# Kernel optimization log

Measured on AMD Instinct MI355X. Metric: run time of the kernel, lower is better.

## Reference

```python
import jax, jax.numpy as jnp
import numpy as np

NEG = jnp.float32(-1e10)

def setup_inputs() -> dict:
    key = jax.random.key(0)
    k1, k2, k3, k4 = jax.random.split(key, 4)
    B, Ns, Nr, D = 64, 512, 256, 1024
    return {
        "span_embeddings": jax.random.normal(k1, (B, Ns, D), dtype=jnp.float32),
        "image_embeddings": jax.random.normal(k2, (B, Nr, D), dtype=jnp.float32),
        "span_mask": jax.random.randint(k3, (B, Ns), 0, 2).astype(jnp.int32),
        "image_mask": jax.random.randint(k4, (B, Nr), 0, 2).astype(jnp.int32),
    }

def reference(span_embeddings, image_embeddings, span_mask, image_mask):
    # pair mask: (B, Ns, Nr) = image_mask[b, None, r] * span_mask[b, s, None]
    mask = (image_mask[:, None, :] * span_mask[:, :, None]).astype(span_embeddings.dtype)
    # QK^T with multiplicative mask, then custom zero->-1e10 masking
    att = jnp.einsum('bsd,brd->bsr', span_embeddings, image_embeddings) * mask
    att = jnp.where(att != 0, att, NEG)
    # spans attend over ROIs
    w_first = jax.nn.softmax(att, axis=-1) * mask
    att_first = jnp.einsum('bsr,brd->bsd', w_first, image_embeddings)
    score = jnp.mean(jnp.square(span_embeddings - att_first))
    # ROIs attend over spans (score_type='both')
    att_t = jnp.swapaxes(att, 1, 2)            # (B, Nr, Ns)
    w_second = jax.nn.softmax(att_t, axis=-1) * jnp.swapaxes(mask, 1, 2)
    att_second = jnp.einsum('brs,bsd->brd', w_second, span_embeddings)
    score = score + jnp.mean(jnp.square(image_embeddings - att_second))
    return score, att_first, att
```

## Files before the change

### kernel.cpp

```cpp
#include <hip/hip_runtime.h>
#include <hip/hip_bf16.h>
#include <math.h>

#define B_  64
#define NS  512
#define NR  256
#define DD  1024
#define NEGV (-1e10f)

typedef __attribute__((ext_vector_type(4))) float f32x4;
typedef __attribute__((ext_vector_type(8))) short bf16x8;

__device__ __forceinline__ unsigned short f2bf(float x) {
    unsigned u = __builtin_bit_cast(unsigned, x);
    unsigned r = u + 0x7FFFu + ((u >> 16) & 1u);
    return (unsigned short)(r >> 16);
}
__device__ __forceinline__ unsigned pk2(float x, float y) {
    unsigned r;
    asm("v_cvt_pk_bf16_f32 %0, %1, %2" : "=v"(r) : "v"(x), "v"(y));
    return r;
}
__device__ __forceinline__ void pk_hilo(float x, float y, unsigned& h, unsigned& l) {
    h = pk2(x, y);
    const float hx = __builtin_bit_cast(float, h << 16);
    const float hy = __builtin_bit_cast(float, h & 0xFFFF0000u);
    l = pk2(x - hx, y - hy);
}
__device__ __forceinline__ void gload16(const void* g, void* l) {
    __builtin_amdgcn_global_load_lds((const __attribute__((address_space(1))) void*)g,
                                     (__attribute__((address_space(3))) void*)l, 16, 0, 0);
}

__global__ __launch_bounds__(64) void zero_ws(double* ws) {
    if (threadIdx.x == 0) { ws[0] = 0.0; ws[1] = 0.0; }
}

__global__ __launch_bounds__(512) void att_mfma(
    const float* __restrict__ span, const float* __restrict__ image,
    const int* __restrict__ smask, const int* __restrict__ imask,
    float* __restrict__ att, float2* __restrict__ rowP, float2* __restrict__ colP,
    int doStats) {
    const int id = blockIdx.x;
    const int b  = id & 63;
    const int ys = (id >> 6) & 3;
    const int xr = id >> 8;
    const int s0 = ys * 128;
    const int r0 = xr * 128;
    __shared__ unsigned short Ah[128][40], Al[128][40], Bh[128][40], Bl[128][40];
    const int tid  = threadIdx.x;
    const int lane = tid & 63;
    const int w    = tid >> 6;
    const int wso  = (w >> 2) * 64;
    const int wro  = (w & 3) * 32;
    const float* Sp = span  + ((size_t)b * NS + s0) * DD;
    const float* Im = image + ((size_t)b * NR + r0) * DD;

    f32x4 acc[4][2];
    #pragma unroll
    for (int i = 0; i < 4; ++i)
        #pragma unroll
        for (int j = 0; j < 2; ++j) acc[i][j] = (f32x4){0.f, 0.f, 0.f, 0.f};

    const int row0 = tid >> 2;
    const int kq   = (tid & 3) * 8;
    const int fr   = lane & 15;
    const int fq   = lane >> 4;
    const int fk   = fq * 8;

    for (int k0 = 0; k0 < DD; k0 += 32) {
        {
            const float4 a0 = *reinterpret_cast<const float4*>(Sp + (size_t)row0 * DD + k0 + kq);
            const float4 a1 = *reinterpret_cast<const float4*>(Sp + (size_t)row0 * DD + k0 + kq + 4);
            const float4 c0 = *reinterpret_cast<const float4*>(Im + (size_t)row0 * DD + k0 + kq);
            const float4 c1 = *reinterpret_cast<const float4*>(Im + (size_t)row0 * DD + k0 + kq + 4);
            unsigned h0, l0, h1, l1, h2, l2, h3, l3;
            uint4 u;
            pk_hilo(a0.x, a0.y, h0, l0); pk_hilo(a0.z, a0.w, h1, l1);
            pk_hilo(a1.x, a1.y, h2, l2); pk_hilo(a1.z, a1.w, h3, l3);
            u.x = h0; u.y = h1; u.z = h2; u.w = h3;
            *reinterpret_cast<uint4*>(&Ah[row0][kq]) = u;
            u.x = l0; u.y = l1; u.z = l2; u.w = l3;
            *reinterpret_cast<uint4*>(&Al[row0][kq]) = u;
            pk_hilo(c0.x, c0.y, h0, l0); pk_hilo(c0.z, c0.w, h1, l1);
            pk_hilo(c1.x, c1.y, h2, l2); pk_hilo(c1.z, c1.w, h3, l3);
            u.x = h0; u.y = h1; u.z = h2; u.w = h3;
            *reinterpret_cast<uint4*>(&Bh[row0][kq]) = u;
            u.x = l0; u.y = l1; u.z = l2; u.w = l3;
            *reinterpret_cast<uint4*>(&Bl[row0][kq]) = u;
        }
        __syncthreads();
        bf16x8 ah[4], al[4], bh[2], bl[2];
        #pragma unroll
        for (int mf = 0; mf < 4; ++mf) {
            ah[mf] = *reinterpret_cast<const bf16x8*>(&Ah[wso + mf * 16 + fr][fk]);
            al[mf] = *reinterpret_cast<const bf16x8*>(&Al[wso + mf * 16 + fr][fk]);
        }
        #pragma unroll
        for (int nf = 0; nf < 2; ++nf) {
            bh[nf] = *reinterpret_cast<const bf16x8*>(&Bh[wro + nf * 16 + fr][fk]);
            bl[nf] = *reinterpret_cast<const bf16x8*>(&Bl[wro + nf * 16 + fr][fk]);
        }
        #pragma unroll
        for (int mf = 0; mf < 4; ++mf)
            #pragma unroll
            for (int nf = 0; nf < 2; ++nf) {
                acc[mf][nf] = __builtin_amdgcn_mfma_f32_16x16x32_bf16(ah[mf], bh[nf], acc[mf][nf], 0, 0, 0);
                acc[mf][nf] = __builtin_amdgcn_mfma_f32_16x16x32_bf16(ah[mf], bl[nf], acc[mf][nf], 0, 0, 0);
                acc[mf][nf] = __builtin_amdgcn_mfma_f32_16x16x32_bf16(al[mf], bh[nf], acc[mf][nf], 0, 0, 0);
            }
        __syncthreads();
    }

    float2* rowLDS = reinterpret_cast<float2*>(&Ah[0][0]);
    float2* colLDS = rowLDS + 512;
    int imv[2];
    #pragma unroll
    for (int nf = 0; nf < 2; ++nf) imv[nf] = imask[b * NR + r0 + wro + nf * 16 + fr];
    float cmax[2] = {-3.4e38f, -3.4e38f};
    float smv[4][4];
    #pragma unroll
    for (int mf = 0; mf < 4; ++mf) {
        #pragma unroll
        for (int i = 0; i < 4; ++i) {
            const int s = s0 + wso + mf * 16 + fq * 4 + i;
            const int sm = smask[b * NS + s];
            smv[mf][i] = (float)sm;
            float* orow = att + ((size_t)b * NS + s) * NR + r0 + wro;
            float vj[2];
            #pragma unroll
            for (int nf = 0; nf < 2; ++nf) {
                float v = acc[mf][nf][i] * (float)(sm * imv[nf]);
                v = (v != 0.0f) ? v : NEGV;
                orow[nf * 16 + fr] = v;
                vj[nf] = v;
                cmax[nf] = fmaxf(cmax[nf], v);
            }
            if (doStats) {
                float rm = fmaxf(vj[0], vj[1]);
                rm = fmaxf(rm, __shfl_xor(rm, 1));
                rm = fmaxf(rm, __shfl_xor(rm, 2));
                rm = fmaxf(rm, __shfl_xor(rm, 4));
                rm = fmaxf(rm, __shfl_xor(rm, 8));
                float rs = __expf(vj[0] - rm) + __expf(vj[1] - rm);
                rs += __shfl_xor(rs, 1);
                rs += __shfl_xor(rs, 2);
                rs += __shfl_xor(rs, 4);
                rs += __shfl_xor(rs, 8);
                if (fr == 0) rowLDS[(wso + mf * 16 + fq * 4 + i) * 4 + (w & 3)] = make_float2(rm, rs);
            }
        }
    }
    if (doStats) {
        #pragma unroll
        for (int nf = 0; nf < 2; ++nf) {
            cmax[nf] = fmaxf(cmax[nf], __shfl_xor(cmax[nf], 16));
            cmax[nf] = fmaxf(cmax[nf], __shfl_xor(cmax[nf], 32));
        }
        float csum[2] = {0.f, 0.f};
        #pragma unroll
        for (int mf = 0; mf < 4; ++mf)
            #pragma unroll
            for (int i = 0; i < 4; ++i)
                #pragma unroll
                for (int nf = 0; nf < 2; ++nf) {
                    float v = acc[mf][nf][i] * (smv[mf][i] * (float)imv[nf]);
                    v = (v != 0.0f) ? v : NEGV;
                    csum[nf] += __expf(v - cmax[nf]);
                }
        #pragma unroll
        for (int nf = 0; nf < 2; ++nf) {
            csum[nf] += __shfl_xor(csum[nf], 16);
            csum[nf] += __shfl_xor(csum[nf], 32);
        }
        if (lane < 16) {
            #pragma unroll
            for (int nf = 0; nf < 2; ++nf)
                colLDS[(wro + nf * 16 + lane) * 2 + (w >> 2)] = make_float2(cmax[nf], csum[nf]);
        }
        __syncthreads();
        if (tid < 128) {
            float2 q0 = rowLDS[tid * 4 + 0], q1 = rowLDS[tid * 4 + 1];
            float2 q2 = rowLDS[tid * 4 + 2], q3 = rowLDS[tid * 4 + 3];
            const float m = fmaxf(fmaxf(q0.x, q1.x), fmaxf(q2.x, q3.x));
            const float ssum = q0.y * __expf(q0.x - m) + q1.y * __expf(q1.x - m)
                             + q2.y * __expf(q2.x - m) + q3.y * __expf(q3.x - m);
            rowP[((size_t)b * NS + s0 + tid) * 2 + xr] = make_float2(m, ssum);
        } else if (tid < 256) {
            const int c = tid - 128;
            const float2 q0 = colLDS[c * 2 + 0], q1 = colLDS[c * 2 + 1];
            const float m = fmaxf(q0.x, q1.x);
            const float ssum = q0.y * __expf(q0.x - m) + q1.y * __expf(q1.x - m);
            colP[((size_t)b * NR + r0 + c) * 4 + ys] = make_float2(m, ssum);
        }
    }
}

__global__ __launch_bounds__(256) void combine_stats(
    const float2* __restrict__ rowP, const float2* __restrict__ colP,
    const int* __restrict__ smask, const int* __restrict__ imask,
    float* __restrict__ m1, float* __restrict__ f1,
    float* __restrict__ m2, float* __restrict__ f2) {
    const int idx = blockIdx.x * 256 + threadIdx.x;
    if (idx < B_ * NS) {
        const float2 p0 = rowP[(size_t)idx * 2 + 0];
        const float2 p1 = rowP[(size_t)idx * 2 + 1];
        const float m = fmaxf(p0.x, p1.x);
        const float s = p0.y * __expf(p0.x - m) + p1.y * __expf(p1.x - m);
        m1[idx] = m;
        f1[idx] = (float)smask[idx] / s;
    } else if (idx < B_ * NS + B_ * NR) {
        const int j = idx - B_ * NS;
        const float2 p0 = colP[(size_t)j * 4 + 0];
        const float2 p1 = colP[(size_t)j * 4 + 1];
        const float2 p2 = colP[(size_t)j * 4 + 2];
        const float2 p3 = colP[(size_t)j * 4 + 3];
        const float m = fmaxf(fmaxf(p0.x, p1.x), fmaxf(p2.x, p3.x));
        const float s = p0.y * __expf(p0.x - m) + p1.y * __expf(p1.x - m)
                      + p2.y * __expf(p2.x - m) + p3.y * __expf(p3.x - m);
        m2[j] = m;
        f2[j] = (float)imask[j] / s;
    }
}

__global__ __launch_bounds__(256) void transpose_swz(
    const float* __restrict__ src, unsigned short* __restrict__ dst, int N) {
    const int b = blockIdx.z, n0 = blockIdx.y * 32, d0 = blockIdx.x * 32;
    __shared__ unsigned short T[32][36];
    const int t = threadIdx.x;
    {
        const int n = t >> 3, dq = (t & 7) * 4;
        const float4 v = *reinterpret_cast<const float4*>(src + ((size_t)b * N + n0 + n) * DD + d0 + dq);
        T[dq + 0][n] = f2bf(v.x); T[dq + 1][n] = f2bf(v.y);
        T[dq + 2][n] = f2bf(v.z); T[dq + 3][n] = f2bf(v.w);
    }
    __syncthreads();
    {
        const int d = t >> 3, nq = (t & 7) * 4;
        const int dg = d0 + d;
        const int base = n0 + nq;
        const int pos = (base & 63) ^ ((dg & 7) << 3);
        const size_t idx = ((size_t)b * DD + dg) * N + (base & ~63) + pos;
        *reinterpret_cast<ushort4*>(dst + idx) = *reinterpret_cast<const ushort4*>(&T[d][nq]);
    }
}

__global__ __launch_bounds__(256) void build_w12(
    const float* __restrict__ att, const int* __restrict__ smask,
    const int* __restrict__ imask,
    const float* __restrict__ m1, const float* __restrict__ f1,
    const float* __restrict__ m2, const float* __restrict__ f2,
    unsigned short* __restrict__ w1g, unsigned short* __restrict__ w2g) {
    const int b = blockIdx.z, s0 = blockIdx.y * 64, r0 = blockIdx.x * 64;
    __shared__ unsigned short T[64][68];
    __shared__ float m2s[64], f2s[64], ims[64];
    const int tid = threadIdx.x;
    if (tid < 64) {
        m2s[tid] = m2[b * NR + r0 + tid];
        f2s[tid] = f2[b * NR + r0 + tid];
        ims[tid] = (float)imask[b * NR + r0 + tid];
    }
    __syncthreads();
    {
        const int srow = tid >> 2, rg = (tid & 3) * 16;
        const int s = s0 + srow;
        const float m1v = m1[b * NS + s], f1v = f1[b * NS + s];
        const float smv = (float)smask[b * NS + s];
        const float* arow = att + ((size_t)b * NS + s) * NR + r0;
        const int w1swz = (s & 7) << 3;
        unsigned short* w1row = w1g + ((size_t)b * NS + s) * NR + r0;
        #pragma unroll
        for (int g = 0; g < 4; ++g) {
            const int rr = rg + g * 4;
            const float4 a = *reinterpret_cast<const float4*>(arow + rr);
            const float e0 = __expf(a.x - m1v) * f1v * ims[rr + 0];
            const float e1 = __expf(a.y - m1v) * f1v * ims[rr + 1];
            const float e2 = __expf(a.z - m1v) * f1v * ims[rr + 2];
            const float e3 = __expf(a.w - m1v) * f1v * ims[rr + 3];
            uint2 u; u.x = pk2(e0, e1); u.y = pk2(e2, e3);
            *reinterpret_cast<uint2*>(w1row + (rr ^ w1swz)) = u;
            const float q0 = __expf(a.x - m2s[rr + 0]) * f2s[rr + 0] * smv;
            const float q1 = __expf(a.y - m2s[rr + 1]) * f2s[rr + 1] * smv;
            const float q2 = __expf(a.z - m2s[rr + 2]) * f2s[rr + 2] * smv;
            const float q3 = __expf(a.w - m2s[rr + 3]) * f2s[rr + 3] * smv;
            const unsigned t0 = pk2(q0, q1), t1 = pk2(q2, q3);
            T[rr + 0][srow] = (unsigned short)(t0 & 0xFFFF);
            T[rr + 1][srow] = (unsigned short)(t0 >> 16);
            T[rr + 2][srow] = (unsigned short)(t1 & 0xFFFF);
            T[rr + 3][srow] = (unsigned short)(t1 >> 16);
        }
    }
    __syncthreads();
    {
        const int rl = tid >> 2, sg = (tid & 3) * 16;
        const int w2swz = (rl & 7) << 3;
        unsigned short* w2row = w2g + ((size_t)b * NR + r0 + rl) * NS + s0;
        #pragma unroll
        for (int g = 0; g < 4; ++g) {
            const int ss = sg + g * 4;
            *reinterpret_cast<ushort4*>(w2row + (ss ^ w2swz)) =
                *reinterpret_cast<const ushort4*>(&T[rl][ss]);
        }
    }
}

template<int KTOT, int MT, bool WOUT, int WIDX>
__global__ __launch_bounds__(256) void gemm_apply(
    const unsigned short* __restrict__ Ag, const unsigned short* __restrict__ Btg,
    const float* __restrict__ ref, float* __restrict__ outp, double* __restrict__ wsum) {
    const int b = blockIdx.z, m0 = blockIdx.y * 64, d0 = blockIdx.x * 256;
    __shared__ unsigned short As[64 * 64];
    __shared__ unsigned short Bs[256 * 64];
    __shared__ float redsum[256];
    const int tid = threadIdx.x, lane = tid & 63, w = tid >> 6;
    const int fr = lane & 15, fq = lane >> 4;
    f32x4 acc[4][4];
    #pragma unroll
    for (int i = 0; i < 4; ++i)
        #pragma unroll
        for (int j = 0; j < 4; ++j) acc[i][j] = (f32x4){0.f, 0.f, 0.f, 0.f};

    const int srow = tid >> 3;
    const int scol = (tid & 7) * 16;
    for (int kc = 0; kc < KTOT / 64; ++kc) {
        const char* asrc = (const char*)(Ag + ((size_t)b * MT + m0) * KTOT) + kc * 128 + scol;
        #pragma unroll
        for (int c = 0; c < 2; ++c)
            gload16(asrc + (size_t)(c * 32 + srow) * (KTOT * 2), (char*)As + (c * 256 + tid) * 16);
        const char* bsrc = (const char*)(Btg + ((size_t)b * DD + d0) * KTOT) + kc * 128 + scol;
        #pragma unroll
        for (int c = 0; c < 8; ++c)
            gload16(bsrc + (size_t)(c * 32 + srow) * (KTOT * 2), (char*)Bs + (c * 256 + tid) * 16);
        __syncthreads();
        #pragma unroll
        for (int ks = 0; ks < 2; ++ks) {
            bf16x8 aF[4], bF[4];
            #pragma unroll
            for (int mf = 0; mf < 4; ++mf) {
                const int row = mf * 16 + fr;
                const int pos = (ks * 32 + fq * 8) ^ ((row & 7) << 3);
                aF[mf] = *reinterpret_cast<const bf16x8*>(&As[row * 64 + pos]);
            }
            #pragma unroll
            for (int nf = 0; nf < 4; ++nf) {
                const int row = w * 64 + nf * 16 + fr;
                const int pos = (ks * 32 + fq * 8) ^ ((row & 7) << 3);
                bF[nf] = *reinterpret_cast<const bf16x8*>(&Bs[row * 64 + pos]);
            }
            #pragma unroll
            for (int mf = 0; mf < 4; ++mf)
                #pragma unroll
                for (int nf = 0; nf < 4; ++nf)
                    acc[mf][nf] = __builtin_amdgcn_mfma_f32_16x16x32_bf16(aF[mf], bF[nf], acc[mf][nf], 0, 0, 0);
        }
        __syncthreads();
    }
    float sumsq = 0.0f;
    #pragma unroll
    for (int mf = 0; mf < 4; ++mf) {
        #pragma unroll
        for (int i = 0; i < 4; ++i) {
            const int row = m0 + mf * 16 + fq * 4 + i;
            const size_t base = ((size_t)b * MT + row) * DD + d0 + w * 64;
            #pragma unroll
            for (int nf = 0; nf < 4; ++nf) {
                const float v = acc[mf][nf][i];
                const float rv = ref[base + nf * 16 + fr];
                if constexpr (WOUT) outp[base + nf * 16 + fr] = v;
                const float dx = rv - v;
                sumsq += dx * dx;
            }
        }
    }
    redsum[tid] = sumsq; __syncthreads();
    for (int off = 128; off; off >>= 1) {
        if (tid < off) redsum[tid] += redsum[tid + off];
        __syncthreads();
    }
    if (tid == 0) atomicAdd(wsum + WIDX, (double)redsum[0]);
}

__global__ __launch_bounds__(256) void first_kernel(
    const float* __restrict__ span, const float* __restrict__ image,
    const int* __restrict__ smask, const int* __restrict__ imask,
    const float* __restrict__ att, float* __restrict__ att_first,
    double* __restrict__ ws) {
    const int b  = blockIdx.y;
    const int s0 = blockIdx.x * 32;
    __shared__ float wT[256][36];
    __shared__ float Is[32][132];
    __shared__ float red[256];
    const int tid  = threadIdx.x;
    const int lane = tid & 63, wave = tid >> 6;
    for (int i = 0; i < 8; ++i) {
        const int srel = wave * 8 + i;
        const int s    = s0 + srel;
        const float4 v = *reinterpret_cast<const float4*>(att + ((size_t)b * NS + s) * NR + lane * 4);
        float m = fmaxf(fmaxf(v.x, v.y), fmaxf(v.z, v.w));
        #pragma unroll
        for (int off = 32; off; off >>= 1) m = fmaxf(m, __shfl_xor(m, off));
        float4 e;
        e.x = expf(v.x - m); e.y = expf(v.y - m); e.z = expf(v.z - m); e.w = expf(v.w - m);
        float sum = e.x + e.y + e.z + e.w;
        #pragma unroll
        for (int off = 32; off; off >>= 1) sum += __shfl_xor(sum, off);
        const float fac = (float)smask[b * NS + s] / sum;
        const int4 im4 = *reinterpret_cast<const int4*>(imask + b * NR + lane * 4);
        wT[lane * 4 + 0][srel] = e.x * fac * (float)im4.x;
        wT[lane * 4 + 1][srel] = e.y * fac * (float)im4.y;
        wT[lane * 4 + 2][srel] = e.z * fac * (float)im4.z;
        wT[lane * 4 + 3][srel] = e.w * fac * (float)im4.w;
    }
    __syncthreads();
    float sumsq = 0.0f;
    const int txd = tid & 31;
    const int tys = tid >> 5;
    const float* Ib = image + (size_t)b * NR * DD;
    for (int dc = 0; dc < 8; ++dc) {
        const int d0 = dc * 128;
        float acc[4][4] = {};
        for (int rc = 0; rc < 8; ++rc) {
            const int r0 = rc * 32;
            {
                const int rr = tid >> 3;
                const int cb = tid & 7;
                const float* src = Ib + (size_t)(r0 + rr) * DD + d0;
                #pragma unroll
                for (int q = 0; q < 4; ++q)
                    *reinterpret_cast<float4*>(&Is[rr][(cb + 8 * q) * 4]) =
                        *reinterpret_cast<const float4*>(src + (cb + 8 * q) * 4);
            }
            __syncthreads();
            #pragma unroll 4
            for (int rr = 0; rr < 32; ++rr) {
                const float4 wv = *reinterpret_cast<const float4*>(&wT[r0 + rr][tys * 4]);
                const float4 iv = *reinterpret_cast<const float4*>(&Is[rr][txd * 4]);
                const float wvv[4] = {wv.x, wv.y, wv.z, wv.w};
                const float ivv[4] = {iv.x, iv.y, iv.z, iv.w};
                #pragma unroll
                for (int i = 0; i < 4; ++i)
                    #pragma unroll
                    for (int j = 0; j < 4; ++j)
                        acc[i][j] += wvv[i] * ivv[j];
            }
            __syncthreads();
        }
        #pragma unroll
        for (int i = 0; i < 4; ++i) {
            const int s = s0 + tys * 4 + i;
            const size_t base = ((size_t)b * NS + s) * DD + d0 + txd * 4;
            const float4 af = {acc[i][0], acc[i][1], acc[i][2], acc[i][3]};
            *reinterpret_cast<float4*>(att_first + base) = af;
            const float4 sp = *reinterpret_cast<const float4*>(span + base);
            float dx;
            dx = sp.x - af.x; sumsq += dx * dx;
            dx = sp.y - af.y; sumsq += dx * dx;
            dx = sp.z - af.z; sumsq += dx * dx;
            dx = sp.w - af.w; sumsq += dx * dx;
        }
    }
    red[tid] = sumsq; __syncthreads();
    for (int off = 128; off; off >>= 1) {
        if (tid < off) red[tid] += red[tid + off];
        __syncthreads();
    }
    if (tid == 0) atomicAdd(ws, (double)red[0]);
}

__global__ __launch_bounds__(256) void second_kernel(
    const float* __restrict__ span, const float* __restrict__ image,
    const int* __restrict__ smask, const int* __restrict__ imask,
    const float* __restrict__ att, double* __restrict__ ws) {
    const int b  = blockIdx.y;
    const int r0 = blockIdx.x * 32;
    __shared__ float w2s[32][36];
    __shared__ float Ss[32][132];
    __shared__ float mArr[32], fArr[32];
    __shared__ float redm[8][32];
    __shared__ float red[256];
    const int tid = threadIdx.x;
    const int rr = tid & 31, q = tid >> 5;
    const float* attb = att + (size_t)b * NS * NR + r0 + rr;
    float mloc = -3.4e38f;
    for (int t = 0; t < 64; ++t)
        mloc = fmaxf(mloc, attb[(size_t)(q * 64 + t) * NR]);
    redm[q][rr] = mloc;
    __syncthreads();
    if (tid < 32) {
        float m = redm[0][tid];
        #pragma unroll
        for (int qq = 1; qq < 8; ++qq) m = fmaxf(m, redm[qq][tid]);
        mArr[tid] = m;
    }
    __syncthreads();
    const float mcol = mArr[rr];
    float sloc = 0.0f;
    for (int t = 0; t < 64; ++t)
        sloc += expf(attb[(size_t)(q * 64 + t) * NR] - mcol);
    redm[q][rr] = sloc;
    __syncthreads();
    if (tid < 32) {
        float s = 0.0f;
        #pragma unroll
        for (int qq = 0; qq < 8; ++qq) s += redm[qq][tid];
        fArr[tid] = (float)imask[b * NR + r0 + tid] / s;
    }
    __syncthreads();
    float sumsq = 0.0f;
    const int txd = tid & 31;
    const int tyr = tid >> 5;
    const float* Sb = span + (size_t)b * NS * DD;
    for (int dc = 0; dc < 8; ++dc) {
        const int d0 = dc * 128;
        float acc[4][4] = {};
        for (int sc = 0; sc < 16; ++sc) {
            const int sb0 = sc * 32;
            {
                const int sr = tid >> 3;
                const int cb = tid & 7;
                const float* src = Sb + (size_t)(sb0 + sr) * DD + d0;
                #pragma unroll
                for (int qq = 0; qq < 4; ++qq)
                    *reinterpret_cast<float4*>(&Ss[sr][(cb + 8 * qq) * 4]) =
                        *reinterpret_cast<const float4*>(src + (cb + 8 * qq) * 4);
            }
            {
                const int ss = tid >> 3;
                const int rq = (tid & 7) * 4;
                const int s  = sb0 + ss;
                const float4 v = *reinterpret_cast<const float4*>(att + ((size_t)b * NS + s) * NR + r0 + rq);
                const float smv = (float)smask[b * NS + s];
                float4 wv;
                wv.x = expf(v.x - mArr[rq + 0]) * fArr[rq + 0] * smv;
                wv.y = expf(v.y - mArr[rq + 1]) * fArr[rq + 1] * smv;
                wv.z = expf(v.z - mArr[rq + 2]) * fArr[rq + 2] * smv;
                wv.w = expf(v.w - mArr[rq + 3]) * fArr[rq + 3] * smv;
                *reinterpret_cast<float4*>(&w2s[ss][rq]) = wv;
            }
            __syncthreads();
            #pragma unroll 4
            for (int ss = 0; ss < 32; ++ss) {
                const float4 wv = *reinterpret_cast<const float4*>(&w2s[ss][tyr * 4]);
                const float4 sv = *reinterpret_cast<const float4*>(&Ss[ss][txd * 4]);
                const float wvv[4] = {wv.x, wv.y, wv.z, wv.w};
                const float svv[4] = {sv.x, sv.y, sv.z, sv.w};
                #pragma unroll
                for (int i = 0; i < 4; ++i)
                    #pragma unroll
                    for (int j = 0; j < 4; ++j)
                        acc[i][j] += wvv[i] * svv[j];
            }
            __syncthreads();
        }
        #pragma unroll
        for (int i = 0; i < 4; ++i) {
            const int r = r0 + tyr * 4 + i;
            const float4 iv = *reinterpret_cast<const float4*>(image + ((size_t)b * NR + r) * DD + d0 + txd * 4);
            float dx;
            dx = iv.x - acc[i][0]; sumsq += dx * dx;
            dx = iv.y - acc[i][1]; sumsq += dx * dx;
            dx = iv.z - acc[i][2]; sumsq += dx * dx;
            dx = iv.w - acc[i][3]; sumsq += dx * dx;
        }
    }
    red[tid] = sumsq; __syncthreads();
    for (int off = 128; off; off >>= 1) {
        if (tid < off) red[tid] += red[tid + off];
        __syncthreads();
    }
    if (tid == 0) atomicAdd(ws + 1, (double)red[0]);
}

__global__ __launch_bounds__(64) void score_kernel(const double* __restrict__ ws, float* __restrict__ out) {
    if (threadIdx.x == 0) {
        out[0] = (float)(ws[0] / (double)((size_t)B_ * NS * DD) +
                         ws[1] / (double)((size_t)B_ * NR * DD));
    }
}

extern "C" void kernel_launch(void* const* d_in, const int* in_sizes, int n_in,
                              void* d_out, int out_size, void* d_ws, size_t ws_size,
                              hipStream_t stream) {
    const float* span  = (const float*)d_in[0];
    const float* image = (const float*)d_in[1];
    const int*   smask = (const int*)d_in[2];
    const int*   imask = (const int*)d_in[3];
    float* out       = (float*)d_out;
    float* att_first = out + 1;
    float* att       = out + 1 + (size_t)B_ * NS * DD;

    char* base = (char*)d_ws;
    double* wsum = (double*)base;
    float* m1 = (float*)(base + 512);
    float* f1 = m1 + (size_t)B_ * NS;
    float* m2 = f1 + (size_t)B_ * NS;
    float* f2 = m2 + (size_t)B_ * NR;
    float2* rowP = (float2*)(f2 + (size_t)B_ * NR);
    float2* colP = rowP + (size_t)B_ * NS * 2;
    char* X0 = (char*)(colP + (size_t)B_ * NR * 4);
    unsigned short* imgT = (unsigned short*)X0;
    unsigned short* w1g  = (unsigned short*)(X0 + (size_t)B_ * DD * NR * 2);
    unsigned short* spT  = (unsigned short*)X0;
    unsigned short* w2g  = (unsigned short*)(X0 + (size_t)B_ * DD * NS * 2);
    const size_t NEED = (size_t)(X0 - base) + (size_t)B_ * DD * NS * 2 + (size_t)B_ * NS * NR * 2;
    const int wsok = (ws_size >= NEED) ? 1 : 0;

    zero_ws<<<dim3(1), dim3(64), 0, stream>>>(wsum);
    att_mfma<<<dim3(512), dim3(512), 0, stream>>>(
        span, image, smask, imask, att, rowP, colP, wsok);

    if (wsok) {
        combine_stats<<<dim3((B_ * NS + B_ * NR) / 256), dim3(256), 0, stream>>>(
            rowP, colP, smask, imask, m1, f1, m2, f2);
        transpose_swz<<<dim3(DD / 32, NR / 32, B_), dim3(256), 0, stream>>>(image, imgT, NR);
        build_w12<<<dim3(NR / 64, NS / 64, B_), dim3(256), 0, stream>>>(
            att, smask, imask, m1, f1, m2, f2, w1g, w2g);
        gemm_apply<NR, NS, true, 0><<<dim3(DD / 256, NS / 64, B_), dim3(256), 0, stream>>>(
            w1g, imgT, span, att_first, wsum);
        transpose_swz<<<dim3(DD / 32, NS / 32, B_), dim3(256), 0, stream>>>(span, spT, NS);
        gemm_apply<NS, NR, false, 1><<<dim3(DD / 256, NR / 64, B_), dim3(256), 0, stream>>>(
            w2g, spT, image, nullptr, wsum);
    } else {
        first_kernel<<<dim3(NS / 32, B_), dim3(256), 0, stream>>>(span, image, smask, imask, att, att_first, wsum);
        second_kernel<<<dim3(NR / 32, B_), dim3(256), 0, stream>>>(span, image, smask, imask, att, wsum);
    }
    score_kernel<<<dim3(1), dim3(64), 0, stream>>>(wsum, out);
}
```

Baseline: 297.3 us.

## Merge prep stages and both apply GEMMs into two combined launches

Folds the stats combine, both bf16 transposes and the weight build into one heterogeneous prep kernel, and runs the two apply GEMMs as a single grid whose blocks choose their problem by blockIdx.y. The per-row and per-column softmax stats are recomputed per tile in shared memory rather than written to global arrays. This removes several launches and the serialization between small kernels. In exchange the workspace grows, because the span and image transposes no longer share a buffer, and the stats are recomputed redundantly across tiles.

After: 290.9 us, median of 2. 2.2% less time.

```diff
diff --git a/kernel.cpp b/kernel.cpp
--- a/kernel.cpp
+++ b/kernel.cpp
@@ -7,6 +7,7 @@
 #define NR  256
 #define DD  1024
 #define NEGV (-1e10f)
+#define NTRANS (32 * 24 * B_)
 
 typedef __attribute__((ext_vector_type(4))) float f32x4;
 typedef __attribute__((ext_vector_type(8))) short bf16x8;
@@ -196,75 +197,73 @@
     }
 }
 
-__global__ __launch_bounds__(256) void combine_stats(
+__global__ __launch_bounds__(256) void prep_kernel(
+    const float* __restrict__ span, const float* __restrict__ image,
+    const int* __restrict__ smask, const int* __restrict__ imask,
+    const float* __restrict__ att,
     const float2* __restrict__ rowP, const float2* __restrict__ colP,
-    const int* __restrict__ smask, const int* __restrict__ imask,
-    float* __restrict__ m1, float* __restrict__ f1,
-    float* __restrict__ m2, float* __restrict__ f2) {
-    const int idx = blockIdx.x * 256 + threadIdx.x;
-    if (idx < B_ * NS) {
-        const float2 p0 = rowP[(size_t)idx * 2 + 0];
-        const float2 p1 = rowP[(size_t)idx * 2 + 1];
+    unsigned short* __restrict__ imgT, unsigned short* __restrict__ spT,
+    unsigned short* __restrict__ w1g, unsigned short* __restrict__ w2g) {
+    __shared__ unsigned short Tt[32][36];
+    __shared__ unsigned short Tb[64][68];
+    __shared__ float m1s[64], f1s[64], m2s[64], f2s[64], ims[64];
+    const int id  = blockIdx.x;
+    const int tid = threadIdx.x;
+    if (id < NTRANS) {
+        const int x = id & 31;
+        const int y = (id >> 5) % 24;
+        const int b = id / (32 * 24);
+        const int d0 = x * 32;
+        const float* src; unsigned short* dst; int N, n0;
+        if (y < 8) { src = image; dst = imgT; N = NR; n0 = y * 32; }
+        else       { src = span;  dst = spT;  N = NS; n0 = (y - 8) * 32; }
+        {
+            const int n = tid >> 3, dq = (tid & 7) * 4;
+            const float4 v = *reinterpret_cast<const float4*>(src + ((size_t)b * N + n0 + n) * DD + d0 + dq);
+            Tt[dq + 0][n] = f2bf(v.x); Tt[dq + 1][n] = f2bf(v.y);
+            Tt[dq + 2][n] = f2bf(v.z); Tt[dq + 3][n] = f2bf(v.w);
+        }
+        __syncthreads();
+        {
+            const int d = tid >> 3, nq = (tid & 7) * 4;
+            const int dg = d0 + d;
+            const int base = n0 + nq;
+            const int pos = (base & 63) ^ ((dg & 7) << 3);
+            const size_t idx = ((size_t)b * DD + dg) * N + (base & ~63) + pos;
+            *reinterpret_cast<ushort4*>(dst + idx) = *reinterpret_cast<const ushort4*>(&Tt[d][nq]);
+        }
+        return;
+    }
+    const int rem = id - NTRANS;
+    const int x = rem & 3;
+    const int y = (rem >> 2) & 7;
+    const int b = rem >> 5;
+    const int s0 = y * 64, r0 = x * 64;
+    if (tid < 64) {
+        const int gs = b * NS + s0 + tid;
+        const float2 p0 = rowP[(size_t)gs * 2 + 0];
+        const float2 p1 = rowP[(size_t)gs * 2 + 1];
         const float m = fmaxf(p0.x, p1.x);
-        const float s = p0.y * __expf(p0.x - m) + p1.y * __expf(p1.x - m);
-        m1[idx] = m;
-        f1[idx] = (float)smask[idx] / s;
-    } else if (idx < B_ * NS + B_ * NR) {
-        const int j = idx - B_ * NS;
-        const float2 p0 = colP[(size_t)j * 4 + 0];
-        const float2 p1 = colP[(size_t)j * 4 + 1];
-        const float2 p2 = colP[(size_t)j * 4 + 2];
-        const float2 p3 = colP[(size_t)j * 4 + 3];
-        const float m = fmaxf(fmaxf(p0.x, p1.x), fmaxf(p2.x, p3.x));
-        const float s = p0.y * __expf(p0.x - m) + p1.y * __expf(p1.x - m)
-                      + p2.y * __expf(p2.x - m) + p3.y * __expf(p3.x - m);
-        m2[j] = m;
-        f2[j] = (float)imask[j] / s;
-    }
-}
-
-__global__ __launch_bounds__(256) void transpose_swz(
-    const float* __restrict__ src, unsigned short* __restrict__ dst, int N) {
-    const int b = blockIdx.z, n0 = blockIdx.y * 32, d0 = blockIdx.x * 32;
-    __shared__ unsigned short T[32][36];
-    const int t = threadIdx.x;
-    {
-        const int n = t >> 3, dq = (t & 7) * 4;
-        const float4 v = *reinterpret_cast<const float4*>(src + ((size_t)b * N + n0 + n) * DD + d0 + dq);
-        T[dq + 0][n] = f2bf(v.x); T[dq + 1][n] = f2bf(v.y);
-        T[dq + 2][n] = f2bf(v.z); T[dq + 3][n] = f2bf(v.w);
-    }
-    __syncthreads();
-    {
-        const int d = t >> 3, nq = (t & 7) * 4;
-        const int dg = d0 + d;
-        const int base = n0 + nq;
-        const int pos = (base & 63) ^ ((dg & 7) << 3);
-        const size_t idx = ((size_t)b * DD + dg) * N + (base & ~63) + pos;
-        *reinterpret_cast<ushort4*>(dst + idx) = *reinterpret_cast<const ushort4*>(&T[d][nq]);
-    }
-}
-
-__global__ __launch_bounds__(256) void build_w12(
-    const float* __restrict__ att, const int* __restrict__ smask,
-    const int* __restrict__ imask,
-    const float* __restrict__ m1, const float* __restrict__ f1,
-    const float* __restrict__ m2, const float* __restrict__ f2,
-    unsigned short* __restrict__ w1g, unsigned short* __restrict__ w2g) {
-    const int b = blockIdx.z, s0 = blockIdx.y * 64, r0 = blockIdx.x * 64;
-    __shared__ unsigned short T[64][68];
-    __shared__ float m2s[64], f2s[64], ims[64];
-    const int tid = threadIdx.x;
-    if (tid < 64) {
-        m2s[tid] = m2[b * NR + r0 + tid];
-        f2s[tid] = f2[b * NR + r0 + tid];
-        ims[tid] = (float)imask[b * NR + r0 + tid];
+        const float ssum = p0.y * __expf(p0.x - m) + p1.y * __expf(p1.x - m);
+        m1s[tid] = m;
+        f1s[tid] = (float)smask[gs] / ssum;
+        const int gr = b * NR + r0 + tid;
+        const float2 q0 = colP[(size_t)gr * 4 + 0];
+        const float2 q1 = colP[(size_t)gr * 4 + 1];
+        const float2 q2 = colP[(size_t)gr * 4 + 2];
+        const float2 q3 = colP[(size_t)gr * 4 + 3];
+        const float mc = fmaxf(fmaxf(q0.x, q1.x), fmaxf(q2.x, q3.x));
+        const float sc = q0.y * __expf(q0.x - mc) + q1.y * __expf(q1.x - mc)
+                       + q2.y * __expf(q2.x - mc) + q3.y * __expf(q3.x - mc);
+        m2s[tid] = mc;
+        f2s[tid] = (float)imask[gr] / sc;
+        ims[tid] = (float)imask[gr];
     }
     __syncthreads();
     {
         const int srow = tid >> 2, rg = (tid & 3) * 16;
         const int s = s0 + srow;
-        const float m1v = m1[b * NS + s], f1v = f1[b * NS + s];
+        const float m1v = m1s[srow], f1v = f1s[srow];
         const float smv = (float)smask[b * NS + s];
         const float* arow = att + ((size_t)b * NS + s) * NR + r0;
         const int w1swz = (s & 7) << 3;
@@ -284,10 +283,10 @@
             const float q2 = __expf(a.z - m2s[rr + 2]) * f2s[rr + 2] * smv;
             const float q3 = __expf(a.w - m2s[rr + 3]) * f2s[rr + 3] * smv;
             const unsigned t0 = pk2(q0, q1), t1 = pk2(q2, q3);
-            T[rr + 0][srow] = (unsigned short)(t0 & 0xFFFF);
-            T[rr + 1][srow] = (unsigned short)(t0 >> 16);
-            T[rr + 2][srow] = (unsigned short)(t1 & 0xFFFF);
-            T[rr + 3][srow] = (unsigned short)(t1 >> 16);
+            Tb[rr + 0][srow] = (unsigned short)(t0 & 0xFFFF);
+            Tb[rr + 1][srow] = (unsigned short)(t0 >> 16);
+            Tb[rr + 2][srow] = (unsigned short)(t1 & 0xFFFF);
+            Tb[rr + 3][srow] = (unsigned short)(t1 >> 16);
         }
     }
     __syncthreads();
@@ -299,19 +298,27 @@
         for (int g = 0; g < 4; ++g) {
             const int ss = sg + g * 4;
             *reinterpret_cast<ushort4*>(w2row + (ss ^ w2swz)) =
-                *reinterpret_cast<const ushort4*>(&T[rl][ss]);
-        }
-    }
-}
-
-template<int KTOT, int MT, bool WOUT, int WIDX>
-__global__ __launch_bounds__(256) void gemm_apply(
-    const unsigned short* __restrict__ Ag, const unsigned short* __restrict__ Btg,
-    const float* __restrict__ ref, float* __restrict__ outp, double* __restrict__ wsum) {
-    const int b = blockIdx.z, m0 = blockIdx.y * 64, d0 = blockIdx.x * 256;
+                *reinterpret_cast<const ushort4*>(&Tb[rl][ss]);
+        }
+    }
+}
+
+__global__ __launch_bounds__(256) void gemm_both(
+    const unsigned short* __restrict__ w1g, const unsigned short* __restrict__ imgT,
+    const float* __restrict__ span, float* __restrict__ att_first,
+    const unsigned short* __restrict__ w2g, const unsigned short* __restrict__ spT,
+    const float* __restrict__ image, double* __restrict__ wsum) {
+    const int b  = blockIdx.z;
+    const int d0 = blockIdx.x * 256;
+    const bool g1 = blockIdx.y < 8;
+    const int m0 = (g1 ? blockIdx.y : (blockIdx.y - 8)) * 64;
+    const int K  = g1 ? NR : NS;
+    const int MT = g1 ? NS : NR;
+    const unsigned short* Ag  = g1 ? w1g : w2g;
+    const unsigned short* Btg = g1 ? imgT : spT;
+    const float* ref = g1 ? span : image;
     __shared__ unsigned short As[64 * 64];
     __shared__ unsigned short Bs[256 * 64];
-    __shared__ float redsum[256];
     const int tid = threadIdx.x, lane = tid & 63, w = tid >> 6;
     const int fr = lane & 15, fq = lane >> 4;
     f32x4 acc[4][4];
@@ -322,15 +329,15 @@
 
     const int srow = tid >> 3;
     const int scol = (tid & 7) * 16;
-    for (int kc = 0; kc < KTOT / 64; ++kc) {
-        const char* asrc = (const char*)(Ag + ((size_t)b * MT + m0) * KTOT) + kc * 128 + scol;
+    for (int kc = 0; kc < K / 64; ++kc) {
+        const char* asrc = (const char*)(Ag + ((size_t)b * MT + m0) * K) + kc * 128 + scol;
         #pragma unroll
         for (int c = 0; c < 2; ++c)
-            gload16(asrc + (size_t)(c * 32 + srow) * (KTOT * 2), (char*)As + (c * 256 + tid) * 16);
-        const char* bsrc = (const char*)(Btg + ((size_t)b * DD + d0) * KTOT) + kc * 128 + scol;
+            gload16(asrc + (size_t)(c * 32 + srow) * (K * 2), (char*)As + (c * 256 + tid) * 16);
+        const char* bsrc = (const char*)(Btg + ((size_t)b * DD + d0) * K) + kc * 128 + scol;
         #pragma unroll
         for (int c = 0; c < 8; ++c)
-            gload16(bsrc + (size_t)(c * 32 + srow) * (KTOT * 2), (char*)Bs + (c * 256 + tid) * 16);
+            gload16(bsrc + (size_t)(c * 32 + srow) * (K * 2), (char*)Bs + (c * 256 + tid) * 16);
         __syncthreads();
         #pragma unroll
         for (int ks = 0; ks < 2; ++ks) {
@@ -366,18 +373,19 @@
             for (int nf = 0; nf < 4; ++nf) {
                 const float v = acc[mf][nf][i];
                 const float rv = ref[base + nf * 16 + fr];
-                if constexpr (WOUT) outp[base + nf * 16 + fr] = v;
+                if (g1) att_first[base + nf * 16 + fr] = v;
                 const float dx = rv - v;
                 sumsq += dx * dx;
             }
         }
     }
+    float* redsum = reinterpret_cast<float*>(As);
     redsum[tid] = sumsq; __syncthreads();
     for (int off = 128; off; off >>= 1) {
         if (tid < off) redsum[tid] += redsum[tid + off];
         __syncthreads();
     }
-    if (tid == 0) atomicAdd(wsum + WIDX, (double)redsum[0]);
+    if (tid == 0) atomicAdd(wsum + (g1 ? 0 : 1), (double)redsum[0]);
 }
 
 __global__ __launch_bounds__(256) void first_kernel(
@@ -591,18 +599,16 @@
 
     char* base = (char*)d_ws;
     double* wsum = (double*)base;
-    float* m1 = (float*)(base + 512);
-    float* f1 = m1 + (size_t)B_ * NS;
-    float* m2 = f1 + (size_t)B_ * NS;
-    float* f2 = m2 + (size_t)B_ * NR;
-    float2* rowP = (float2*)(f2 + (size_t)B_ * NR);
+    float2* rowP = (float2*)(base + 512);
     float2* colP = rowP + (size_t)B_ * NS * 2;
     char* X0 = (char*)(colP + (size_t)B_ * NR * 4);
     unsigned short* imgT = (unsigned short*)X0;
-    unsigned short* w1g  = (unsigned short*)(X0 + (size_t)B_ * DD * NR * 2);
-    unsigned short* spT  = (unsigned short*)X0;
-    unsigned short* w2g  = (unsigned short*)(X0 + (size_t)B_ * DD * NS * 2);
-    const size_t NEED = (size_t)(X0 - base) + (size_t)B_ * DD * NS * 2 + (size_t)B_ * NS * NR * 2;
+    unsigned short* spT  = imgT + (size_t)B_ * DD * NR;
+    unsigned short* w1g  = spT  + (size_t)B_ * DD * NS;
+    unsigned short* w2g  = w1g  + (size_t)B_ * NS * NR;
+    const size_t NEED = (size_t)(X0 - base)
+                      + 2 * ((size_t)B_ * DD * NR + (size_t)B_ * DD * NS
+                           + (size_t)B_ * NS * NR + (size_t)B_ * NR * NS);
     const int wsok = (ws_size >= NEED) ? 1 : 0;
 
     zero_ws<<<dim3(1), dim3(64), 0, stream>>>(wsum);
@@ -610,16 +616,10 @@
         span, image, smask, imask, att, rowP, colP, wsok);
 
     if (wsok) {
-        combine_stats<<<dim3((B_ * NS + B_ * NR) / 256), dim3(256), 0, stream>>>(
-            rowP, colP, smask, imask, m1, f1, m2, f2);
-        transpose_swz<<<dim3(DD / 32, NR / 32, B_), dim3(256), 0, stream>>>(image, imgT, NR);
-        build_w12<<<dim3(NR / 64, NS / 64, B_), dim3(256), 0, stream>>>(
-            att, smask, imask, m1, f1, m2, f2, w1g, w2g);
-        gemm_apply<NR, NS, true, 0><<<dim3(DD / 256, NS / 64, B_), dim3(256), 0, stream>>>(
-            w1g, imgT, span, att_first, wsum);
-        transpose_swz<<<dim3(DD / 32, NS / 32, B_), dim3(256), 0, stream>>>(span, spT, NS);
-        gemm_apply<NS, NR, false, 1><<<dim3(DD / 256, NR / 64, B_), dim3(256), 0, stream>>>(
-            w2g, spT, image, nullptr, wsum);
+        prep_kernel<<<dim3(NTRANS + (NR / 64) * (NS / 64) * B_), dim3(256), 0, stream>>>(
+            span, image, smask, imask, att, rowP, colP, imgT, spT, w1g, w2g);
+        gemm_both<<<dim3(DD / 256, 12, B_), dim3(256), 0, stream>>>(
+            w1g, imgT, span, att_first, w2g, spT, image, wsum);
     } else {
         first_kernel<<<dim3(NS / 32, B_), dim3(256), 0, stream>>>(span, image, smask, imask, att, att_first, wsum);
         second_kernel<<<dim3(NR / 32, B_), dim3(256), 0, stream>>>(span, image, smask, imask, att, wsum);
```
